# Kernel tuning notes

Hardware: AMD Instinct MI355X
Metric: run time of the kernel (lower is better)

The kernel has to match this reference:

```python
import jax, jax.numpy as jnp
import numpy as np

N, T, LLM_DIM, HID, E = 50000, 8, 256, 128, 800000


def setup_inputs() -> dict:
    key = jax.random.key(0)
    ks = jax.random.split(key, 16)
    s = 0.05
    return {
        "x": jax.random.normal(ks[0], (N, T, LLM_DIM), dtype=jnp.float32),
        "edge_index": jax.random.randint(ks[1], (2, E), 0, N, dtype=jnp.int32),
        "edge_weight": jax.random.uniform(ks[2], (E,), dtype=jnp.float32),
        "att_c_W": jax.random.normal(ks[3], (LLM_DIM, HID), dtype=jnp.float32) * s,
        "att_c_b": jax.random.normal(ks[4], (HID,), dtype=jnp.float32) * s,
        "att_c_v": jax.random.normal(ks[5], (HID,), dtype=jnp.float32) * s,
        "att_o_W": jax.random.normal(ks[6], (LLM_DIM, HID), dtype=jnp.float32) * s,
        "att_o_b": jax.random.normal(ks[7], (HID,), dtype=jnp.float32) * s,
        "att_o_v": jax.random.normal(ks[8], (HID,), dtype=jnp.float32) * s,
        "Wc": jax.random.normal(ks[9], (LLM_DIM, HID), dtype=jnp.float32) * s,
        "bc": jax.random.normal(ks[10], (HID,), dtype=jnp.float32) * s,
        "Wo": jax.random.normal(ks[11], (LLM_DIM, HID), dtype=jnp.float32) * s,
        "bo": jax.random.normal(ks[12], (HID,), dtype=jnp.float32) * s,
    }


def _attention(x, W, b, v):
    # x: [N, T, D] -> pooled [N, D] via additive attention over tokens
    e = jnp.einsum("nth,h->nt", jnp.tanh(jnp.einsum("ntd,dh->nth", x, W) + b), v)
    a = jax.nn.softmax(e, axis=-1)  # [N, T]
    return jnp.einsum("nt,ntd->nd", a, x)


def _lgconv(x, src, dst, w, n_nodes):
    # gather -> edge-weight multiply -> scatter-add (LGConv with given edge_weight)
    msg = x[src] * w[:, None]  # [E, D]
    return jax.ops.segment_sum(msg, dst, num_segments=n_nodes)


def _gnn(x, src, dst, w, n_nodes):
    x = _lgconv(x, src, dst, w, n_nodes)
    x = _lgconv(x, src, dst, w, n_nodes)
    return x


def reference(x, edge_index, edge_weight, att_c_W, att_c_b, att_c_v,
              att_o_W, att_o_b, att_o_v, Wc, bc, Wo, bo):
    n_nodes = x.shape[0]
    src, dst = edge_index[0], edge_index[1]
    c = _attention(x, att_c_W, att_c_b, att_c_v)  # [N, D]
    o = _attention(x, att_o_W, att_o_b, att_o_v)  # [N, D]
    c = _gnn(c, src, dst, edge_weight, n_nodes) + c
    o = _gnn(o, src, dst, edge_weight, n_nodes) + o
    center = c @ Wc + bc
    offset = jax.nn.relu(o @ Wo + bo)
    return center, offset
```

## Files before the change

kernel.cpp:

```cpp
#include <hip/hip_runtime.h>
#include <hip/hip_bf16.h>
#include <cstdint>

#define NN 50000
#define TT 8
#define DD 256
#define HH 128
#define EE 800000
#define CAP 64

typedef float f32x4 __attribute__((ext_vector_type(4)));
typedef short s16x8 __attribute__((ext_vector_type(8)));
typedef char  s8x8  __attribute__((ext_vector_type(8)));

struct __align__(16) ERec { int s; float w; float w1; float w2; };

__device__ inline unsigned short f2bf(float f) {
    __bf16 b = (__bf16)f;
    return *reinterpret_cast<unsigned short*>(&b);
}
__device__ inline float bf2f(unsigned short h) {
    union { unsigned u; float f; } c; c.u = ((unsigned)h) << 16;
    return c.f;
}

__global__ __launch_bounds__(256) void k_prew(
    const float* __restrict__ Wac, const float* __restrict__ Wao,
    const float* __restrict__ Wc,  const float* __restrict__ Wo,
    short* __restrict__ Bsw1, short* __restrict__ Bsw2,
    int* __restrict__ cursor)
{
    if (blockIdx.x < 64) {
        int t = blockIdx.x * 256 + threadIdx.x;
        int mat = t >> 13;
        int r = t & 8191;
        int kt = r >> 10;
        int ct = (r >> 6) & 15;
        int lane = r & 63;
        int g = lane >> 4, lr = lane & 15;
        const float* W = mat ? (ct < 8 ? Wc : Wo) : (ct < 8 ? Wac : Wao);
        int c = (ct & 7) * 16 + lr;
        short* out = (mat ? Bsw2 : Bsw1) + ((size_t)((kt * 16 + ct) * 64 + lane)) * 8;
        #pragma unroll
        for (int j = 0; j < 8; ++j) {
            int k = kt * 32 + g * 8 + j;
            out[j] = (short)f2bf(W[k * HH + c]);
        }
    } else {
        int i = (blockIdx.x - 64) * 256 + threadIdx.x;
        if (i < NN) cursor[i] = 0;
    }
}

__global__ __launch_bounds__(256, 3) void k_att5(
    const float* __restrict__ x,
    const short* __restrict__ Bsw1, const short* __restrict__ Bsw2,
    const float* __restrict__ bac, const float* __restrict__ vac,
    const float* __restrict__ bao, const float* __restrict__ vao,
    unsigned short* __restrict__ cpo_bf, char* __restrict__ cpo_q, float* __restrict__ cpo_s)
{
    __shared__ __align__(16) char smem[34304];
    short* xs = (short*)smem;
    float* part   = (float*)(smem + 32768);
    float* av_lds = (float*)(smem + 33792);
    short* PL = (short*)smem;
    unsigned short* cob = (unsigned short*)(smem + 8192);

    const int tid = threadIdx.x;
    const int w = tid >> 6, lane = tid & 63;
    const int lr = lane & 15, g = lane >> 4;
    const int h = w >> 1;

    {
        const float* xb = x + (size_t)blockIdx.x * (64 * 256);
        #pragma unroll
        for (int half = 0; half < 2; ++half) {
            float4 va[4], vb[4];
            #pragma unroll
            for (int k = 0; k < 4; ++k) {
                int u = (half * 4 + k) * 256 + tid;
                const float4* p = (const float4*)(xb + (size_t)u * 8);
                va[k] = p[0]; vb[k] = p[1];
            }
            #pragma unroll
            for (int k = 0; k < 4; ++k) {
                int u = (half * 4 + k) * 256 + tid;
                int row = u >> 5, cu = u & 31;
                s16x8 s;
                s[0] = (short)f2bf(va[k].x); s[1] = (short)f2bf(va[k].y);
                s[2] = (short)f2bf(va[k].z); s[3] = (short)f2bf(va[k].w);
                s[4] = (short)f2bf(vb[k].x); s[5] = (short)f2bf(vb[k].y);
                s[6] = (short)f2bf(vb[k].z); s[7] = (short)f2bf(vb[k].w);
                int byte = row * 512 + ((cu * 16) ^ ((row & 7) << 4));
                *(s16x8*)((char*)xs + byte) = s;
            }
        }
    }
    __syncthreads();

    float ep[4][4];
    #pragma unroll
    for (int rt = 0; rt < 4; ++rt)
        #pragma unroll
        for (int i = 0; i < 4; ++i) ep[rt][i] = 0.f;

    const s16x8* B1 = (const s16x8*)Bsw1;
    const int sw = (lr & 7) << 4;
    #pragma unroll
    for (int p = 0; p < 2; ++p) {
        const int ct0 = w * 4 + p * 2;
        s16x8 b0[8], b1[8];
        #pragma unroll
        for (int kt = 0; kt < 8; ++kt) {
            b0[kt] = B1[(kt * 16 + ct0) * 64 + lane];
            b1[kt] = B1[(kt * 16 + ct0 + 1) * 64 + lane];
        }
        const int jj0 = (w & 1) * 64 + p * 32 + lr;
        const float bb0 = h ? bao[jj0] : bac[jj0];
        const float vv0 = h ? vao[jj0] : vac[jj0];
        const float bb1 = h ? bao[jj0 + 16] : bac[jj0 + 16];
        const float vv1 = h ? vao[jj0 + 16] : vac[jj0 + 16];
        #pragma unroll
        for (int rt = 0; rt < 4; ++rt) {
            char* base = (char*)xs + (rt * 16 + lr) * 512;
            f32x4 acc0 = {0.f, 0.f, 0.f, 0.f}, acc1 = {0.f, 0.f, 0.f, 0.f};
            #pragma unroll
            for (int kt = 0; kt < 8; ++kt) {
                s16x8 a = *(const s16x8*)(base + ((kt * 64 + g * 16) ^ sw));
                acc0 = __builtin_amdgcn_mfma_f32_16x16x32_bf16(a, b0[kt], acc0, 0, 0, 0);
                acc1 = __builtin_amdgcn_mfma_f32_16x16x32_bf16(a, b1[kt], acc1, 0, 0, 0);
            }
            #pragma unroll
            for (int i = 0; i < 4; ++i) {
                float e0 = __expf(2.f * (acc0[i] + bb0));
                float t0 = (e0 - 1.f) * __builtin_amdgcn_rcpf(e0 + 1.f);
                float e1 = __expf(2.f * (acc1[i] + bb1));
                float t1 = (e1 - 1.f) * __builtin_amdgcn_rcpf(e1 + 1.f);
                ep[rt][i] += t0 * vv0 + t1 * vv1;
            }
        }
    }

    #pragma unroll
    for (int rt = 0; rt < 4; ++rt)
        #pragma unroll
        for (int i = 0; i < 4; ++i) {
            float v = ep[rt][i];
            v += __shfl_xor(v, 1); v += __shfl_xor(v, 2);
            v += __shfl_xor(v, 4); v += __shfl_xor(v, 8);
            ep[rt][i] = v;
        }
    if (lr == 0) {
        #pragma unroll
        for (int rt = 0; rt < 4; ++rt)
            #pragma unroll
            for (int i = 0; i < 4; ++i)
                part[w * 64 + rt * 16 + g * 4 + i] = ep[rt][i];
    }
    __syncthreads();

    if (tid < 128) {
        int hh = tid >> 6, row = tid & 63, nb = row & ~7;
        float ee[8];
        #pragma unroll
        for (int u = 0; u < 8; ++u)
            ee[u] = part[hh * 128 + nb + u] + part[hh * 128 + 64 + nb + u];
        float m = -1e30f;
        #pragma unroll
        for (int u = 0; u < 8; ++u) m = fmaxf(m, ee[u]);
        float s = 0.f;
        #pragma unroll
        for (int u = 0; u < 8; ++u) s += __expf(ee[u] - m);
        av_lds[hh * 64 + row] = __expf(ee[row & 7] - m) * __builtin_amdgcn_rcpf(s);
    }
    __syncthreads();

    float accp[2][4][2];
    const int d2 = tid & 127;
    const int nb = (tid >> 7) * 4;
    {
        #pragma unroll
        for (int hh = 0; hh < 2; ++hh)
            #pragma unroll
            for (int nn = 0; nn < 4; ++nn) { accp[hh][nn][0] = 0.f; accp[hh][nn][1] = 0.f; }
        #pragma unroll
        for (int nn = 0; nn < 4; ++nn) {
            const int n = nb + nn;
            #pragma unroll
            for (int t = 0; t < 8; ++t) {
                int row = n * 8 + t;
                unsigned u = *(const unsigned*)((char*)xs + row * 512 + ((d2 * 4) ^ (t << 4)));
                float lo = bf2f((unsigned short)(u & 0xffff));
                float hi = bf2f((unsigned short)(u >> 16));
                float a0 = av_lds[row], a1 = av_lds[64 + row];
                accp[0][nn][0] = fmaf(a0, lo, accp[0][nn][0]);
                accp[0][nn][1] = fmaf(a0, hi, accp[0][nn][1]);
                accp[1][nn][0] = fmaf(a1, lo, accp[1][nn][0]);
                accp[1][nn][1] = fmaf(a1, hi, accp[1][nn][1]);
            }
        }
    }
    __syncthreads();

    {
        int col = d2 * 2;
        int kt = col >> 5, gg = (col >> 3) & 3, jp = col & 7;
        #pragma unroll
        for (int hh = 0; hh < 2; ++hh)
            #pragma unroll
            for (int nn = 0; nn < 4; ++nn) {
                int n = nb + nn;
                unsigned pv = (unsigned)f2bf(accp[hh][nn][0]) | ((unsigned)f2bf(accp[hh][nn][1]) << 16);
                int sidx = (((hh * 8 + kt) * 4 + gg) * 8 + n) * 8 + jp;
                *(unsigned*)((char*)PL + sidx * 2) = pv;
            }
    }
    __syncthreads();

    {
        const int head = w >> 1;
        s16x8 a2[8];
        #pragma unroll
        for (int kt = 0; kt < 8; ++kt) {
            int sidx = (((head * 8 + kt) * 4 + g) * 8 + (lr & 7)) * 8;
            a2[kt] = *(const s16x8*)((char*)PL + sidx * 2);
        }
        const s16x8* B2 = (const s16x8*)Bsw2;
        #pragma unroll
        for (int c2 = 0; c2 < 4; ++c2) {
            int ct = w * 4 + c2;
            f32x4 acc = {0.f, 0.f, 0.f, 0.f};
            #pragma unroll
            for (int kt = 0; kt < 8; ++kt)
                acc = __builtin_amdgcn_mfma_f32_16x16x32_bf16(a2[kt], B2[(kt * 16 + ct) * 64 + lane], acc, 0, 0, 0);
            if (g < 2) {
                int col = head * 128 + (ct & 7) * 16 + lr;
                #pragma unroll
                for (int i = 0; i < 4; ++i) {
                    int node = g * 4 + i;
                    cob[node * 256 + col] = f2bf(acc[i]);
                }
            }
        }
    }
    __syncthreads();

    {
        const int n0 = blockIdx.x * 8;
        const int row = tid >> 5;
        s16x8 cb = *(const s16x8*)&cob[row * 256 + (tid & 31) * 8];
        float v[8]; float m = 0.f;
        #pragma unroll
        for (int j = 0; j < 8; ++j) { v[j] = bf2f((unsigned short)cb[j]); m = fmaxf(m, fabsf(v[j])); }
        #pragma unroll
        for (int d = 1; d < 32; d <<= 1) m = fmaxf(m, __shfl_xor(m, d));
        float inv = (m > 0.f) ? 127.f / m : 0.f;
        s8x8 q;
        #pragma unroll
        for (int j = 0; j < 8; ++j) q[j] = (char)__float2int_rn(v[j] * inv);
        const size_t base = (size_t)n0 * 256;
        ((s16x8*)(cpo_bf + base))[tid] = cb;
        ((s8x8*)(cpo_q + base))[tid] = q;
        if ((tid & 31) == 0) cpo_s[n0 + row] = m * (1.f / 127.f);
    }
}

__global__ void k_fill(const int* __restrict__ src, const int* __restrict__ dst,
                       const float* __restrict__ w,
                       int* __restrict__ cursor, ERec* __restrict__ erec,
                       const float* __restrict__ cpo_s) {
    int e = blockIdx.x * 256 + threadIdx.x;
    if (e >= EE) return;
    int s = src[e];
    int d = dst[e];
    float wt = w[e];
    int pos = atomicAdd(&cursor[d], 1);
    if (pos < CAP) {
        ERec r; r.s = s; r.w = wt; r.w1 = wt * cpo_s[s]; r.w2 = 0.f;
        erec[d * CAP + pos] = r;
    }
}

__global__ __launch_bounds__(256) void k_ew2(
    int* __restrict__ cursor, ERec* __restrict__ erec, const float* __restrict__ g1_s)
{
    const int lane = threadIdx.x & 63;
    const int node = blockIdx.x * 4 + (threadIdx.x >> 6);
    int cnt = min(cursor[node], CAP);
    if (lane < cnt) {
        ERec* r = &erec[node * CAP + lane];
        r->w2 = r->w * g1_s[r->s];
    }
}

__global__ __launch_bounds__(256) void k_hop1(
    const char* __restrict__ cpo_q,
    const int* __restrict__ cursor, const ERec* __restrict__ erec,
    char* __restrict__ g1_q, float* __restrict__ g1_s)
{
    const int lane = threadIdx.x & 63;
    const int node = blockIdx.x * 4 + (threadIdx.x >> 6);
    const int half = lane >> 5;
    const int c0 = (lane & 31) * 8;
    const int s0 = node * CAP;
    const int s1 = s0 + min(cursor[node], CAP);
    float acc[8] = {0.f, 0.f, 0.f, 0.f, 0.f, 0.f, 0.f, 0.f};
    int i = s0 + half;
    for (; i + 6 < s1; i += 8) {
        ERec e0 = erec[i], e1 = erec[i + 2], e2 = erec[i + 4], e3 = erec[i + 6];
        s8x8 v0 = *(const s8x8*)&cpo_q[(size_t)e0.s * 256 + c0];
        s8x8 v1 = *(const s8x8*)&cpo_q[(size_t)e1.s * 256 + c0];
        s8x8 v2 = *(const s8x8*)&cpo_q[(size_t)e2.s * 256 + c0];
        s8x8 v3 = *(const s8x8*)&cpo_q[(size_t)e3.s * 256 + c0];
        #pragma unroll
        for (int j = 0; j < 8; ++j) {
            acc[j] = fmaf(e0.w1, (float)v0[j],
                     fmaf(e1.w1, (float)v1[j],
                     fmaf(e2.w1, (float)v2[j],
                     fmaf(e3.w1, (float)v3[j], acc[j]))));
        }
    }
    for (; i < s1; i += 2) {
        ERec e0 = erec[i];
        s8x8 v0 = *(const s8x8*)&cpo_q[(size_t)e0.s * 256 + c0];
        #pragma unroll
        for (int j = 0; j < 8; ++j)
            acc[j] = fmaf(e0.w1, (float)v0[j], acc[j]);
    }
    #pragma unroll
    for (int j = 0; j < 8; ++j) acc[j] += __shfl_xor(acc[j], 32);
    float m = 0.f;
    #pragma unroll
    for (int j = 0; j < 8; ++j) m = fmaxf(m, fabsf(acc[j]));
    #pragma unroll
    for (int d = 1; d < 32; d <<= 1) m = fmaxf(m, __shfl_xor(m, d));
    if (half == 0) {
        float inv = (m > 0.f) ? 127.f / m : 0.f;
        s8x8 q;
        #pragma unroll
        for (int j = 0; j < 8; ++j) q[j] = (char)__float2int_rn(acc[j] * inv);
        *(s8x8*)&g1_q[(size_t)node * 256 + c0] = q;
        if (lane == 0) g1_s[node] = m * (1.f / 127.f);
    }
}

__global__ __launch_bounds__(256) void k_hop2(
    const char* __restrict__ g1_q,
    const unsigned short* __restrict__ cpo_bf,
    const float* __restrict__ bc, const float* __restrict__ bo,
    const int* __restrict__ cursor, const ERec* __restrict__ erec,
    float* __restrict__ out)
{
    const int lane = threadIdx.x & 63;
    const int node = blockIdx.x * 4 + (threadIdx.x >> 6);
    const int half = lane >> 5;
    const int c0 = (lane & 31) * 8;
    const int s0 = node * CAP;
    const int s1 = s0 + min(cursor[node], CAP);
    float acc[8] = {0.f, 0.f, 0.f, 0.f, 0.f, 0.f, 0.f, 0.f};
    int i = s0 + half;
    for (; i + 6 < s1; i += 8) {
        ERec e0 = erec[i], e1 = erec[i + 2], e2 = erec[i + 4], e3 = erec[i + 6];
        s8x8 v0 = *(const s8x8*)&g1_q[(size_t)e0.s * 256 + c0];
        s8x8 v1 = *(const s8x8*)&g1_q[(size_t)e1.s * 256 + c0];
        s8x8 v2 = *(const s8x8*)&g1_q[(size_t)e2.s * 256 + c0];
        s8x8 v3 = *(const s8x8*)&g1_q[(size_t)e3.s * 256 + c0];
        #pragma unroll
        for (int j = 0; j < 8; ++j) {
            acc[j] = fmaf(e0.w2, (float)v0[j],
                     fmaf(e1.w2, (float)v1[j],
                     fmaf(e2.w2, (float)v2[j],
                     fmaf(e3.w2, (float)v3[j], acc[j]))));
        }
    }
    for (; i < s1; i += 2) {
        ERec e0 = erec[i];
        s8x8 v0 = *(const s8x8*)&g1_q[(size_t)e0.s * 256 + c0];
        #pragma unroll
        for (int j = 0; j < 8; ++j)
            acc[j] = fmaf(e0.w2, (float)v0[j], acc[j]);
    }
    #pragma unroll
    for (int j = 0; j < 8; ++j) acc[j] += __shfl_xor(acc[j], 32);
    if (half == 0) {
        s16x8 cv = *(const s16x8*)&cpo_bf[(size_t)node * 256 + c0];
        float r[8];
        if (c0 < 128) {
            #pragma unroll
            for (int j = 0; j < 8; ++j)
                r[j] = acc[j] + bf2f((unsigned short)cv[j]) + bc[c0 + j];
            float4* o4 = (float4*)&out[(size_t)node * 128 + c0];
            o4[0] = make_float4(r[0], r[1], r[2], r[3]);
            o4[1] = make_float4(r[4], r[5], r[6], r[7]);
        } else {
            #pragma unroll
            for (int j = 0; j < 8; ++j)
                r[j] = fmaxf(acc[j] + bf2f((unsigned short)cv[j]) + bo[c0 - 128 + j], 0.f);
            float4* o4 = (float4*)&out[(size_t)NN * 128 + (size_t)node * 128 + (c0 - 128)];
            o4[0] = make_float4(r[0], r[1], r[2], r[3]);
            o4[1] = make_float4(r[4], r[5], r[6], r[7]);
        }
    }
}

extern "C" void kernel_launch(void* const* d_in, const int* in_sizes, int n_in,
                              void* d_out, int out_size, void* d_ws, size_t ws_size,
                              hipStream_t stream)
{
    const float* x   = (const float*)d_in[0];
    const int*   ei  = (const int*)d_in[1];
    const float* ew  = (const float*)d_in[2];
    const float* Wac = (const float*)d_in[3];
    const float* bac = (const float*)d_in[4];
    const float* vac = (const float*)d_in[5];
    const float* Wao = (const float*)d_in[6];
    const float* bao = (const float*)d_in[7];
    const float* vao = (const float*)d_in[8];
    const float* Wc  = (const float*)d_in[9];
    const float* bc  = (const float*)d_in[10];
    const float* Wo  = (const float*)d_in[11];
    const float* bo  = (const float*)d_in[12];
    float* out = (float*)d_out;

    char* ws = (char*)d_ws;
    unsigned short* cpo_bf = (unsigned short*)(ws + 0);
    char*  cpo_q  = (char*)(ws + 25600000);
    float* cpo_s  = (float*)(ws + 38400000);
    char*  g1_q   = (char*)(ws + 38600192);
    float* g1_s   = (float*)(ws + 51400192);
    short* Bsw1   = (short*)(ws + 51600384);
    short* Bsw2   = (short*)(ws + 51731456);
    int*   cursor = (int*)(ws + 51862528);
    ERec*  erec   = (ERec*)(ws + 52062720);

    const int* src = ei;
    const int* dst = ei + EE;

    k_prew<<<64 + (NN + 255) / 256, 256, 0, stream>>>(Wac, Wao, Wc, Wo, Bsw1, Bsw2, cursor);
    k_att5<<<NN / 8, 256, 0, stream>>>(x, Bsw1, Bsw2, bac, vac, bao, vao, cpo_bf, cpo_q, cpo_s);
    k_fill<<<(EE + 255) / 256, 256, 0, stream>>>(src, dst, ew, cursor, erec, cpo_s);
    k_hop1<<<NN / 4, 256, 0, stream>>>(cpo_q, cursor, erec, g1_q, g1_s);
    k_ew2<<<NN / 4, 256, 0, stream>>>(cursor, erec, g1_s);
    k_hop2<<<NN / 4, 256, 0, stream>>>(g1_q, cpo_bf, bc, bo, cursor, erec, out);
}
```

Baseline: 298.8 us.

## Make attention kernel persistent over chunks with register prefetch of next tile

The attention kernel now processes 8 chunks of 8 nodes per block instead of one, prefetching the next chunk's x tile into registers while the current chunk's pooling and output GEMM run. The aim is to hide global load latency for the large x read and cut block launch overhead. The cost is 64 extra VGPRs for the prefetch buffer under a 3-blocks-per-CU launch bound, which may cause spills or lower occupancy. The grid also shrinks to about 782 blocks, which can leave the GPU's CUs less evenly loaded.

```diff
diff --git a/kernel.cpp b/kernel.cpp
--- a/kernel.cpp
+++ b/kernel.cpp
@@ -8,6 +8,8 @@
 #define HH 128
 #define EE 800000
 #define CAP 64
+#define NCH 6250
+#define CPB 8
 
 typedef float f32x4 __attribute__((ext_vector_type(4)));
 typedef short s16x8 __attribute__((ext_vector_type(8)));
@@ -52,7 +54,7 @@
     }
 }
 
-__global__ __launch_bounds__(256, 3) void k_att5(
+__global__ __launch_bounds__(256, 3) void k_att6(
     const float* __restrict__ x,
     const short* __restrict__ Bsw1, const short* __restrict__ Bsw2,
     const float* __restrict__ bac, const float* __restrict__ vac,
@@ -70,198 +72,215 @@
     const int w = tid >> 6, lane = tid & 63;
     const int lr = lane & 15, g = lane >> 4;
     const int h = w >> 1;
-
+    const int sw = (lr & 7) << 4;
+
+    const int chunk0 = blockIdx.x * CPB;
+
+    float4 pf[16];
     {
-        const float* xb = x + (size_t)blockIdx.x * (64 * 256);
-        #pragma unroll
-        for (int half = 0; half < 2; ++half) {
-            float4 va[4], vb[4];
-            #pragma unroll
-            for (int k = 0; k < 4; ++k) {
-                int u = (half * 4 + k) * 256 + tid;
+        const float* xb = x + (size_t)chunk0 * (64 * 256);
+        #pragma unroll
+        for (int k = 0; k < 8; ++k) {
+            int u = k * 256 + tid;
+            const float4* p = (const float4*)(xb + (size_t)u * 8);
+            pf[2 * k] = p[0]; pf[2 * k + 1] = p[1];
+        }
+    }
+
+    for (int c = 0; c < CPB; ++c) {
+        const int chunk = chunk0 + c;
+        if (chunk >= NCH) break;
+
+        #pragma unroll
+        for (int k = 0; k < 8; ++k) {
+            int u = k * 256 + tid;
+            int row = u >> 5, cu = u & 31;
+            float4 va = pf[2 * k], vb = pf[2 * k + 1];
+            s16x8 s;
+            s[0] = (short)f2bf(va.x); s[1] = (short)f2bf(va.y);
+            s[2] = (short)f2bf(va.z); s[3] = (short)f2bf(va.w);
+            s[4] = (short)f2bf(vb.x); s[5] = (short)f2bf(vb.y);
+            s[6] = (short)f2bf(vb.z); s[7] = (short)f2bf(vb.w);
+            int byte = row * 512 + ((cu * 16) ^ ((row & 7) << 4));
+            *(s16x8*)((char*)xs + byte) = s;
+        }
+        __syncthreads();
+
+        float ep[4][4];
+        #pragma unroll
+        for (int rt = 0; rt < 4; ++rt)
+            #pragma unroll
+            for (int i = 0; i < 4; ++i) ep[rt][i] = 0.f;
+
+        const s16x8* B1 = (const s16x8*)Bsw1;
+        #pragma unroll
+        for (int p = 0; p < 2; ++p) {
+            const int ct0 = w * 4 + p * 2;
+            s16x8 b0[8], b1[8];
+            #pragma unroll
+            for (int kt = 0; kt < 8; ++kt) {
+                b0[kt] = B1[(kt * 16 + ct0) * 64 + lane];
+                b1[kt] = B1[(kt * 16 + ct0 + 1) * 64 + lane];
+            }
+            const int jj0 = (w & 1) * 64 + p * 32 + lr;
+            const float bb0 = h ? bao[jj0] : bac[jj0];
+            const float vv0 = h ? vao[jj0] : vac[jj0];
+            const float bb1 = h ? bao[jj0 + 16] : bac[jj0 + 16];
+            const float vv1 = h ? vao[jj0 + 16] : vac[jj0 + 16];
+            #pragma unroll
+            for (int rt = 0; rt < 4; ++rt) {
+                char* base = (char*)xs + (rt * 16 + lr) * 512;
+                f32x4 acc0 = {0.f, 0.f, 0.f, 0.f}, acc1 = {0.f, 0.f, 0.f, 0.f};
+                #pragma unroll
+                for (int kt = 0; kt < 8; ++kt) {
+                    s16x8 a = *(const s16x8*)(base + ((kt * 64 + g * 16) ^ sw));
+                    acc0 = __builtin_amdgcn_mfma_f32_16x16x32_bf16(a, b0[kt], acc0, 0, 0, 0);
+                    acc1 = __builtin_amdgcn_mfma_f32_16x16x32_bf16(a, b1[kt], acc1, 0, 0, 0);
+                }
+                #pragma unroll
+                for (int i = 0; i < 4; ++i) {
+                    float e0 = __expf(2.f * (acc0[i] + bb0));
+                    float t0 = (e0 - 1.f) * __builtin_amdgcn_rcpf(e0 + 1.f);
+                    float e1 = __expf(2.f * (acc1[i] + bb1));
+                    float t1 = (e1 - 1.f) * __builtin_amdgcn_rcpf(e1 + 1.f);
+                    ep[rt][i] += t0 * vv0 + t1 * vv1;
+                }
+            }
+        }
+
+        #pragma unroll
+        for (int rt = 0; rt < 4; ++rt)
+            #pragma unroll
+            for (int i = 0; i < 4; ++i) {
+                float v = ep[rt][i];
+                v += __shfl_xor(v, 1); v += __shfl_xor(v, 2);
+                v += __shfl_xor(v, 4); v += __shfl_xor(v, 8);
+                ep[rt][i] = v;
+            }
+        if (lr == 0) {
+            #pragma unroll
+            for (int rt = 0; rt < 4; ++rt)
+                #pragma unroll
+                for (int i = 0; i < 4; ++i)
+                    part[w * 64 + rt * 16 + g * 4 + i] = ep[rt][i];
+        }
+        __syncthreads();
+
+        if (tid < 128) {
+            int hh = tid >> 6, row = tid & 63, nb = row & ~7;
+            float ee[8];
+            #pragma unroll
+            for (int u = 0; u < 8; ++u)
+                ee[u] = part[hh * 128 + nb + u] + part[hh * 128 + 64 + nb + u];
+            float m = -1e30f;
+            #pragma unroll
+            for (int u = 0; u < 8; ++u) m = fmaxf(m, ee[u]);
+            float s = 0.f;
+            #pragma unroll
+            for (int u = 0; u < 8; ++u) s += __expf(ee[u] - m);
+            av_lds[hh * 64 + row] = __expf(ee[row & 7] - m) * __builtin_amdgcn_rcpf(s);
+        }
+        __syncthreads();
+
+        float accp[2][4][2];
+        const int d2 = tid & 127;
+        const int nb = (tid >> 7) * 4;
+        {
+            #pragma unroll
+            for (int hh = 0; hh < 2; ++hh)
+                #pragma unroll
+                for (int nn = 0; nn < 4; ++nn) { accp[hh][nn][0] = 0.f; accp[hh][nn][1] = 0.f; }
+            #pragma unroll
+            for (int nn = 0; nn < 4; ++nn) {
+                const int n = nb + nn;
+                #pragma unroll
+                for (int t = 0; t < 8; ++t) {
+                    int row = n * 8 + t;
+                    unsigned u = *(const unsigned*)((char*)xs + row * 512 + ((d2 * 4) ^ (t << 4)));
+                    float lo = bf2f((unsigned short)(u & 0xffff));
+                    float hi = bf2f((unsigned short)(u >> 16));
+                    float a0 = av_lds[row], a1 = av_lds[64 + row];
+                    accp[0][nn][0] = fmaf(a0, lo, accp[0][nn][0]);
+                    accp[0][nn][1] = fmaf(a0, hi, accp[0][nn][1]);
+                    accp[1][nn][0] = fmaf(a1, lo, accp[1][nn][0]);
+                    accp[1][nn][1] = fmaf(a1, hi, accp[1][nn][1]);
+                }
+            }
+        }
+        __syncthreads();
+
+        if (c + 1 < CPB && chunk + 1 < NCH) {
+            const float* xb = x + (size_t)(chunk + 1) * (64 * 256);
+            #pragma unroll
+            for (int k = 0; k < 8; ++k) {
+                int u = k * 256 + tid;
                 const float4* p = (const float4*)(xb + (size_t)u * 8);
-                va[k] = p[0]; vb[k] = p[1];
-            }
-            #pragma unroll
-            for (int k = 0; k < 4; ++k) {
-                int u = (half * 4 + k) * 256 + tid;
-                int row = u >> 5, cu = u & 31;
-                s16x8 s;
-                s[0] = (short)f2bf(va[k].x); s[1] = (short)f2bf(va[k].y);
-                s[2] = (short)f2bf(va[k].z); s[3] = (short)f2bf(va[k].w);
-                s[4] = (short)f2bf(vb[k].x); s[5] = (short)f2bf(vb[k].y);
-                s[6] = (short)f2bf(vb[k].z); s[7] = (short)f2bf(vb[k].w);
-                int byte = row * 512 + ((cu * 16) ^ ((row & 7) << 4));
-                *(s16x8*)((char*)xs + byte) = s;
-            }
-        }
-    }
-    __syncthreads();
-
-    float ep[4][4];
-    #pragma unroll
-    for (int rt = 0; rt < 4; ++rt)
-        #pragma unroll
-        for (int i = 0; i < 4; ++i) ep[rt][i] = 0.f;
-
-    const s16x8* B1 = (const s16x8*)Bsw1;
-    const int sw = (lr & 7) << 4;
-    #pragma unroll
-    for (int p = 0; p < 2; ++p) {
-        const int ct0 = w * 4 + p * 2;
-        s16x8 b0[8], b1[8];
-        #pragma unroll
-        for (int kt = 0; kt < 8; ++kt) {
-            b0[kt] = B1[(kt * 16 + ct0) * 64 + lane];
-            b1[kt] = B1[(kt * 16 + ct0 + 1) * 64 + lane];
-        }
-        const int jj0 = (w & 1) * 64 + p * 32 + lr;
-        const float bb0 = h ? bao[jj0] : bac[jj0];
-        const float vv0 = h ? vao[jj0] : vac[jj0];
-        const float bb1 = h ? bao[jj0 + 16] : bac[jj0 + 16];
-        const float vv1 = h ? vao[jj0 + 16] : vac[jj0 + 16];
-        #pragma unroll
-        for (int rt = 0; rt < 4; ++rt) {
-            char* base = (char*)xs + (rt * 16 + lr) * 512;
-            f32x4 acc0 = {0.f, 0.f, 0.f, 0.f}, acc1 = {0.f, 0.f, 0.f, 0.f};
+                pf[2 * k] = p[0]; pf[2 * k + 1] = p[1];
+            }
+        }
+
+        {
+            int col = d2 * 2;
+            int kt = col >> 5, gg = (col >> 3) & 3, jp = col & 7;
+            #pragma unroll
+            for (int hh = 0; hh < 2; ++hh)
+                #pragma unroll
+                for (int nn = 0; nn < 4; ++nn) {
+                    int n = nb + nn;
+                    unsigned pv = (unsigned)f2bf(accp[hh][nn][0]) | ((unsigned)f2bf(accp[hh][nn][1]) << 16);
+                    int sidx = (((hh * 8 + kt) * 4 + gg) * 8 + n) * 8 + jp;
+                    *(unsigned*)((char*)PL + sidx * 2) = pv;
+                }
+        }
+        __syncthreads();
+
+        {
+            const int head = w >> 1;
+            s16x8 a2[8];
             #pragma unroll
             for (int kt = 0; kt < 8; ++kt) {
-                s16x8 a = *(const s16x8*)(base + ((kt * 64 + g * 16) ^ sw));
-                acc0 = __builtin_amdgcn_mfma_f32_16x16x32_bf16(a, b0[kt], acc0, 0, 0, 0);
-                acc1 = __builtin_amdgcn_mfma_f32_16x16x32_bf16(a, b1[kt], acc1, 0, 0, 0);
-            }
-            #pragma unroll
-            for (int i = 0; i < 4; ++i) {
-                float e0 = __expf(2.f * (acc0[i] + bb0));
-                float t0 = (e0 - 1.f) * __builtin_amdgcn_rcpf(e0 + 1.f);
-                float e1 = __expf(2.f * (acc1[i] + bb1));
-                float t1 = (e1 - 1.f) * __builtin_amdgcn_rcpf(e1 + 1.f);
-                ep[rt][i] += t0 * vv0 + t1 * vv1;
-            }
-        }
-    }
-
-    #pragma unroll
-    for (int rt = 0; rt < 4; ++rt)
-        #pragma unroll
-        for (int i = 0; i < 4; ++i) {
-            float v = ep[rt][i];
-            v += __shfl_xor(v, 1); v += __shfl_xor(v, 2);
-            v += __shfl_xor(v, 4); v += __shfl_xor(v, 8);
-            ep[rt][i] = v;
-        }
-    if (lr == 0) {
-        #pragma unroll
-        for (int rt = 0; rt < 4; ++rt)
-            #pragma unroll
-            for (int i = 0; i < 4; ++i)
-                part[w * 64 + rt * 16 + g * 4 + i] = ep[rt][i];
-    }
-    __syncthreads();
-
-    if (tid < 128) {
-        int hh = tid >> 6, row = tid & 63, nb = row & ~7;
-        float ee[8];
-        #pragma unroll
-        for (int u = 0; u < 8; ++u)
-            ee[u] = part[hh * 128 + nb + u] + part[hh * 128 + 64 + nb + u];
-        float m = -1e30f;
-        #pragma unroll
-        for (int u = 0; u < 8; ++u) m = fmaxf(m, ee[u]);
-        float s = 0.f;
-        #pragma unroll
-        for (int u = 0; u < 8; ++u) s += __expf(ee[u] - m);
-        av_lds[hh * 64 + row] = __expf(ee[row & 7] - m) * __builtin_amdgcn_rcpf(s);
-    }
-    __syncthreads();
-
-    float accp[2][4][2];
-    const int d2 = tid & 127;
-    const int nb = (tid >> 7) * 4;
-    {
-        #pragma unroll
-        for (int hh = 0; hh < 2; ++hh)
-            #pragma unroll
-            for (int nn = 0; nn < 4; ++nn) { accp[hh][nn][0] = 0.f; accp[hh][nn][1] = 0.f; }
-        #pragma unroll
-        for (int nn = 0; nn < 4; ++nn) {
-            const int n = nb + nn;
-            #pragma unroll
-            for (int t = 0; t < 8; ++t) {
-                int row = n * 8 + t;
-                unsigned u = *(const unsigned*)((char*)xs + row * 512 + ((d2 * 4) ^ (t << 4)));
-                float lo = bf2f((unsigned short)(u & 0xffff));
-                float hi = bf2f((unsigned short)(u >> 16));
-                float a0 = av_lds[row], a1 = av_lds[64 + row];
-                accp[0][nn][0] = fmaf(a0, lo, accp[0][nn][0]);
-                accp[0][nn][1] = fmaf(a0, hi, accp[0][nn][1]);
-                accp[1][nn][0] = fmaf(a1, lo, accp[1][nn][0]);
-                accp[1][nn][1] = fmaf(a1, hi, accp[1][nn][1]);
-            }
-        }
-    }
-    __syncthreads();
-
-    {
-        int col = d2 * 2;
-        int kt = col >> 5, gg = (col >> 3) & 3, jp = col & 7;
-        #pragma unroll
-        for (int hh = 0; hh < 2; ++hh)
-            #pragma unroll
-            for (int nn = 0; nn < 4; ++nn) {
-                int n = nb + nn;
-                unsigned pv = (unsigned)f2bf(accp[hh][nn][0]) | ((unsigned)f2bf(accp[hh][nn][1]) << 16);
-                int sidx = (((hh * 8 + kt) * 4 + gg) * 8 + n) * 8 + jp;
-                *(unsigned*)((char*)PL + sidx * 2) = pv;
-            }
-    }
-    __syncthreads();
-
-    {
-        const int head = w >> 1;
-        s16x8 a2[8];
-        #pragma unroll
-        for (int kt = 0; kt < 8; ++kt) {
-            int sidx = (((head * 8 + kt) * 4 + g) * 8 + (lr & 7)) * 8;
-            a2[kt] = *(const s16x8*)((char*)PL + sidx * 2);
-        }
-        const s16x8* B2 = (const s16x8*)Bsw2;
-        #pragma unroll
-        for (int c2 = 0; c2 < 4; ++c2) {
-            int ct = w * 4 + c2;
-            f32x4 acc = {0.f, 0.f, 0.f, 0.f};
-            #pragma unroll
-            for (int kt = 0; kt < 8; ++kt)
-                acc = __builtin_amdgcn_mfma_f32_16x16x32_bf16(a2[kt], B2[(kt * 16 + ct) * 64 + lane], acc, 0, 0, 0);
-            if (g < 2) {
-                int col = head * 128 + (ct & 7) * 16 + lr;
-                #pragma unroll
-                for (int i = 0; i < 4; ++i) {
-                    int node = g * 4 + i;
-                    cob[node * 256 + col] = f2bf(acc[i]);
+                int sidx = (((head * 8 + kt) * 4 + g) * 8 + (lr & 7)) * 8;
+                a2[kt] = *(const s16x8*)((char*)PL + sidx * 2);
+            }
+            const s16x8* B2 = (const s16x8*)Bsw2;
+            #pragma unroll
+            for (int c2 = 0; c2 < 4; ++c2) {
+                int ct = w * 4 + c2;
+                f32x4 acc = {0.f, 0.f, 0.f, 0.f};
+                #pragma unroll
+                for (int kt = 0; kt < 8; ++kt)
+                    acc = __builtin_amdgcn_mfma_f32_16x16x32_bf16(a2[kt], B2[(kt * 16 + ct) * 64 + lane], acc, 0, 0, 0);
+                if (g < 2) {
+                    int col = head * 128 + (ct & 7) * 16 + lr;
+                    #pragma unroll
+                    for (int i = 0; i < 4; ++i) {
+                        int node = g * 4 + i;
+                        cob[node * 256 + col] = f2bf(acc[i]);
+                    }
                 }
             }
         }
-    }
-    __syncthreads();
-
-    {
-        const int n0 = blockIdx.x * 8;
-        const int row = tid >> 5;
-        s16x8 cb = *(const s16x8*)&cob[row * 256 + (tid & 31) * 8];
-        float v[8]; float m = 0.f;
-        #pragma unroll
-        for (int j = 0; j < 8; ++j) { v[j] = bf2f((unsigned short)cb[j]); m = fmaxf(m, fabsf(v[j])); }
-        #pragma unroll
-        for (int d = 1; d < 32; d <<= 1) m = fmaxf(m, __shfl_xor(m, d));
-        float inv = (m > 0.f) ? 127.f / m : 0.f;
-        s8x8 q;
-        #pragma unroll
-        for (int j = 0; j < 8; ++j) q[j] = (char)__float2int_rn(v[j] * inv);
-        const size_t base = (size_t)n0 * 256;
-        ((s16x8*)(cpo_bf + base))[tid] = cb;
-        ((s8x8*)(cpo_q + base))[tid] = q;
-        if ((tid & 31) == 0) cpo_s[n0 + row] = m * (1.f / 127.f);
+        __syncthreads();
+
+        {
+            const int n0 = chunk * 8;
+            const int row = tid >> 5;
+            s16x8 cb = *(const s16x8*)&cob[row * 256 + (tid & 31) * 8];
+            float v[8]; float m = 0.f;
+            #pragma unroll
+            for (int j = 0; j < 8; ++j) { v[j] = bf2f((unsigned short)cb[j]); m = fmaxf(m, fabsf(v[j])); }
+            #pragma unroll
+            for (int d = 1; d < 32; d <<= 1) m = fmaxf(m, __shfl_xor(m, d));
+            float inv = (m > 0.f) ? 127.f / m : 0.f;
+            s8x8 q;
+            #pragma unroll
+            for (int j = 0; j < 8; ++j) q[j] = (char)__float2int_rn(v[j] * inv);
+            const size_t base = (size_t)n0 * 256;
+            ((s16x8*)(cpo_bf + base))[tid] = cb;
+            ((s8x8*)(cpo_q + base))[tid] = q;
+            if ((tid & 31) == 0) cpo_s[n0 + row] = m * (1.f / 127.f);
+        }
+        __syncthreads();
     }
 }
 
@@ -437,7 +456,7 @@
     const int* dst = ei + EE;
 
     k_prew<<<64 + (NN + 255) / 256, 256, 0, stream>>>(Wac, Wao, Wc, Wo, Bsw1, Bsw2, cursor);
-    k_att5<<<NN / 8, 256, 0, stream>>>(x, Bsw1, Bsw2, bac, vac, bao, vao, cpo_bf, cpo_q, cpo_s);
+    k_att6<<<(NCH + CPB - 1) / CPB, 256, 0, stream>>>(x, Bsw1, Bsw2, bac, vac, bao, vao, cpo_bf, cpo_q, cpo_s);
     k_fill<<<(EE + 255) / 256, 256, 0, stream>>>(src, dst, ew, cursor, erec, cpo_s);
     k_hop1<<<NN / 4, 256, 0, stream>>>(cpo_q, cursor, erec, g1_q, g1_s);
     k_ew2<<<NN / 4, 256, 0, stream>>>(cursor, erec, g1_s);
```

Result: slower. 824.7 us (+176.0%).
